# Kernel tuning notes

Measured on AMD Instinct MI355X. Metric: run time of the kernel, lower is better.

## Reference

```python
import jax, jax.numpy as jnp
import numpy as np
import math

FACTOR = 5


def setup_inputs() -> dict:
    key = jax.random.key(0)
    k1, k2, k3, k4 = jax.random.split(key, 4)
    B, L, H, D = 8, 1024, 8, 64
    S = FACTOR * math.ceil(math.log(L))  # U_part = 35
    return {
        "queries": jax.random.normal(k1, (B, L, H, D), jnp.float32),
        "keys": jax.random.normal(k2, (B, L, H, D), jnp.float32),
        "values": jax.random.normal(k3, (B, L, H, D), jnp.float32),
        "sample_idx": jax.random.randint(k4, (L, S), 0, L, dtype=jnp.int32),
        "attn_mask": 0,  # unused by the original forward
    }


def reference(queries, keys, values, sample_idx, attn_mask):
    B, L_Q, H, D = queries.shape
    L_K = keys.shape[1]
    # [B, L, H, D] -> [B, H, L, D]
    Q = jnp.transpose(queries, (0, 2, 1, 3))
    K = jnp.transpose(keys, (0, 2, 1, 3))
    V = jnpp_transpose(values) if False else jnp.transpose(values, (0, 2, 1, 3))

    u = min(FACTOR * math.ceil(math.log(L_Q)), L_Q)  # n_top

    # --- _prob_QK: sampled scores, sparsity measure, top-u query selection ---
    K_sample = K[:, :, sample_idx, :]  # [B, H, L_Q, S, D]
    QK_sample = jnp.einsum('bhqd,bhqsd->bhqs', Q, K_sample)  # [B, H, L_Q, S]
    M = QK_sample.max(axis=-1) - QK_sample.sum(axis=-1) / L_K  # [B, H, L_Q]
    _, M_top = jax.lax.top_k(M, u)  # [B, H, u]

    Q_reduce = jnp.take_along_axis(Q, M_top[..., None], axis=2)  # [B, H, u, D]
    scale = 1.0 / math.sqrt(D)
    scores_top = jnp.einsum('bhud,bhkd->bhuk', Q_reduce, K) * scale  # [B, H, u, L_K]

    # --- initial context (mask_flag=True): running causal mean of V ---
    denom = jnp.arange(1, L_K + 1, dtype=V.dtype)[:, None]  # [L_K, 1]
    context = jnp.cumsum(V, axis=2) / denom  # [B, H, L_K, D]

    # --- softmax over keys, sparse update of selected query rows ---
    attn = jax.nn.softmax(scores_top, axis=-1)  # [B, H, u, L_K]
    update = jnp.einsum('bhuk,bhkd->bhud', attn, V)  # [B, H, u, D]

    b_idx = jnp.arange(B)[:, None, None]
    h_idx = jnp.arange(H)[None, :, None]
    context = context.at[b_idx, h_idx, M_top].set(update)

    return jnp.transpose(context, (0, 2, 1, 3))  # [B, L_Q, H, D]
```

## Files before the change

kernel.cpp:

```cpp
#include <hip/hip_runtime.h>
#include <math.h>

#define BB 8
#define LL 1024
#define HH 8
#define DD 64
#define SS 35
#define UU 35
#define BH (BB*HH)
#define NCHK 4
#define CHK 256
#define RPAD 48

#define CSBLOCKS BH
#define MBLOCKS (BB*LL)

typedef __attribute__((ext_vector_type(8))) short short8;
typedef __attribute__((ext_vector_type(4))) float f32x4;

__device__ __forceinline__ size_t qkv_off(int b, int l, int h, int d) {
    return (((size_t)b*LL + l)*HH + h)*DD + d;
}

__device__ __forceinline__ unsigned short f2bf(float x) {
    unsigned int u = __float_as_uint(x);
    u = (u + 0x7fffu + ((u >> 16) & 1u)) >> 16;
    return (unsigned short)u;
}

__device__ __forceinline__ short8 ld_bf8_g(const float* __restrict__ p) {
    float4 x = *reinterpret_cast<const float4*>(p);
    float4 y = *reinterpret_cast<const float4*>(p + 4);
    short8 r;
    r[0] = (short)f2bf(x.x); r[1] = (short)f2bf(x.y);
    r[2] = (short)f2bf(x.z); r[3] = (short)f2bf(x.w);
    r[4] = (short)f2bf(y.x); r[5] = (short)f2bf(y.y);
    r[6] = (short)f2bf(y.z); r[7] = (short)f2bf(y.w);
    return r;
}

__device__ __forceinline__ void gload_lds16(const void* g, void* l) {
    __builtin_amdgcn_global_load_lds(
        (const __attribute__((address_space(1))) void*)g,
        (__attribute__((address_space(3))) void*)l, 16, 0, 0);
}

__device__ __forceinline__ float red8_shr(float p) {
    int t;
    t = __builtin_amdgcn_update_dpp(0, __float_as_int(p), 0x111, 0xF, 0xF, true);
    p += __int_as_float(t);
    t = __builtin_amdgcn_update_dpp(0, __float_as_int(p), 0x112, 0xF, 0xF, true);
    p += __int_as_float(t);
    t = __builtin_amdgcn_update_dpp(0, __float_as_int(p), 0x114, 0xF, 0xF, true);
    p += __int_as_float(t);
    return p;
}

__device__ __forceinline__ float wave_fmax64(float x) {
    int t;
    t = __builtin_amdgcn_update_dpp(0, __float_as_int(x), 0xB1, 0xF, 0xF, true);
    x = fmaxf(x, __int_as_float(t));
    t = __builtin_amdgcn_update_dpp(0, __float_as_int(x), 0x4E, 0xF, 0xF, true);
    x = fmaxf(x, __int_as_float(t));
    t = __builtin_amdgcn_update_dpp(0, __float_as_int(x), 0x141, 0xF, 0xF, true);
    x = fmaxf(x, __int_as_float(t));
    t = __builtin_amdgcn_update_dpp(0, __float_as_int(x), 0x140, 0xF, 0xF, true);
    x = fmaxf(x, __int_as_float(t));
    x = fmaxf(x, __shfl_xor(x, 16));
    x = fmaxf(x, __shfl_xor(x, 32));
    return x;
}

__device__ __forceinline__ int wave_imin64(int x) {
    int t;
    t = __builtin_amdgcn_update_dpp(0, x, 0xB1, 0xF, 0xF, true);  x = (t < x) ? t : x;
    t = __builtin_amdgcn_update_dpp(0, x, 0x4E, 0xF, 0xF, true);  x = (t < x) ? t : x;
    t = __builtin_amdgcn_update_dpp(0, x, 0x141, 0xF, 0xF, true); x = (t < x) ? t : x;
    t = __builtin_amdgcn_update_dpp(0, x, 0x140, 0xF, 0xF, true); x = (t < x) ? t : x;
    int y;
    y = __shfl_xor(x, 16); x = (y < x) ? y : x;
    y = __shfl_xor(x, 32); x = (y < x) ? y : x;
    return x;
}

__global__ __launch_bounds__(256, 3) void kernel_M_cumsum(const float* __restrict__ Q,
                                                          const float* __restrict__ K,
                                                          const float* __restrict__ V,
                                                          const int*   __restrict__ sidx,
                                                          float* __restrict__ M,
                                                          float* __restrict__ out) {
    int blk = blockIdx.x;
    if (blk < CSBLOCKS) {
        __shared__ float partial[4][64];
        int bh = blk;
        int b = bh >> 3, h = bh & 7;
        int d = threadIdx.x & 63, seg = threadIdx.x >> 6;
        int l0 = seg * 256;
        const float* vp = V + qkv_off(b, l0, h, d);

        float s = 0.f;
#pragma unroll 8
        for (int i = 0; i < 256; i++) s += vp[(size_t)i * (HH * DD)];
        partial[seg][d] = s;
        __syncthreads();
        float run = 0.f;
#pragma unroll
        for (int ss = 0; ss < 3; ss++) {
            float v = partial[ss][d];
            run += (ss < seg) ? v : 0.f;
        }
        float* op = out + qkv_off(b, l0, h, d);
#pragma unroll 8
        for (int i = 0; i < 256; i++) {
            run += vp[(size_t)i * (HH * DD)];
            op[(size_t)i * (HH * DD)] = run / (float)(l0 + i + 1);
        }
    } else {
        __shared__ float rows[4 * 2560];
        __shared__ float s_mx[4][8];
        __shared__ float s_sm[4][8];
        int mblk = blk - CSBLOCKS;
        int b = mblk & 7;
        int q = mblk >> 3;
        int tid = threadIdx.x;
        int w = tid >> 6, lane = tid & 63;
        int h = lane >> 3, j = lane & 7;

        const float* qb = Q + ((size_t)(b * LL + q) * HH + h) * DD + j * 4;
        f32x4 q0 = *reinterpret_cast<const f32x4*>(qb);
        f32x4 q1 = *reinterpret_cast<const f32x4*>(qb + 32);

        const int* sq = sidx + q * SS + w * 9;
        const char* kb = (const char*)(K + (size_t)b * (LL * HH * DD));
        char* region = (char*)(rows + w * 2560);
        const float* region_f = rows + w * 2560;

        float mx = -INFINITY, sm = 0.f;

        {
            int sl[5];
#pragma unroll
            for (int i = 0; i < 5; i++) sl[i] = sq[i];
#pragma unroll
            for (int r = 0; r < 5; r++) {
                const char* gsrc = kb + (size_t)sl[r] * 2048 + lane * 16;
                gload_lds16(gsrc,        region + r * 2048);
                gload_lds16(gsrc + 1024, region + r * 2048 + 1024);
            }
            asm volatile("s_waitcnt vmcnt(0)" ::: "memory");
#pragma unroll
            for (int r = 0; r < 5; r++) {
                const float* rp = region_f + r * 512 + h * 64 + j * 4;
                f32x4 k0 = *reinterpret_cast<const f32x4*>(rp);
                f32x4 k1 = *reinterpret_cast<const f32x4*>(rp + 32);
                float d = q0.x * k0.x + q0.y * k0.y + q0.z * k0.z + q0.w * k0.w
                        + q1.x * k1.x + q1.y * k1.y + q1.z * k1.z + q1.w * k1.w;
                d = red8_shr(d);
                mx = fmaxf(mx, d); sm += d;
            }
            asm volatile("s_waitcnt lgkmcnt(0)" ::: "memory");
        }

        {
            int sl[4];
#pragma unroll
            for (int i = 0; i < 4; i++) {
                int ii = (i == 3 && w == 3) ? 2 : i;
                sl[i] = sq[5 + ii];
            }
#pragma unroll
            for (int r = 0; r < 4; r++) {
                const char* gsrc = kb + (size_t)sl[r] * 2048 + lane * 16;
                gload_lds16(gsrc,        region + r * 2048);
                gload_lds16(gsrc + 1024, region + r * 2048 + 1024);
            }
            asm volatile("s_waitcnt vmcnt(0)" ::: "memory");
#pragma unroll
            for (int r = 0; r < 4; r++) {
                const float* rp = region_f + r * 512 + h * 64 + j * 4;
                f32x4 k0 = *reinterpret_cast<const f32x4*>(rp);
                f32x4 k1 = *reinterpret_cast<const f32x4*>(rp + 32);
                float d = q0.x * k0.x + q0.y * k0.y + q0.z * k0.z + q0.w * k0.w
                        + q1.x * k1.x + q1.y * k1.y + q1.z * k1.z + q1.w * k1.w;
                d = red8_shr(d);
                bool valid = (r < 3) || (w < 3);
                if (valid) { mx = fmaxf(mx, d); sm += d; }
            }
        }

        if (j == 7) { s_mx[w][h] = mx; s_sm[w][h] = sm; }
        __syncthreads();
        if (tid < 8) {
            float m2 = -INFINITY, s2 = 0.f;
#pragma unroll
            for (int ww = 0; ww < 4; ww++) {
                m2 = fmaxf(m2, s_mx[ww][tid]);
                s2 += s_sm[ww][tid];
            }
            M[(b * HH + tid) * LL + q] = m2 - s2 * (1.0f / LL);
        }
    }
}

__global__ __launch_bounds__(64, 4) void kernel_topk(const float* __restrict__ M,
                                                     int* __restrict__ top) {
    int bh = blockIdx.x, lane = threadIdx.x;
    float v[16];
#pragma unroll
    for (int i = 0; i < 16; i++) v[i] = M[bh * LL + i * 64 + lane];

    for (int k = 0; k < UU; k++) {
        float bv = -INFINITY; int bslot = 0;
#pragma unroll
        for (int i = 0; i < 16; i++) {
            if (v[i] > bv) { bv = v[i]; bslot = i; }
        }
        float wm = wave_fmax64(bv);
        int gidx = (bv == wm) ? (bslot * 64 + lane) : 0x7fffffff;
        int widx = wave_imin64(gidx);
        if (lane == 0) top[bh * UU + k] = widx;
        if ((widx & 63) == lane) {
            int slot = widx >> 6;
#pragma unroll
            for (int i = 0; i < 16; i++) if (i == slot) v[i] = -INFINITY;
        }
    }
}

__global__ __launch_bounds__(256) void kernel_attn_part(const float* __restrict__ Q,
                                                        const float* __restrict__ K,
                                                        const float* __restrict__ V,
                                                        const int*   __restrict__ top,
                                                        float* __restrict__ m_ws,
                                                        float* __restrict__ se_ws,
                                                        float* __restrict__ pv_ws) {
    __shared__ unsigned short vt[64 * CHK];
    __shared__ unsigned short p_lds[RPAD * CHK];
    __shared__ float red_m[4][RPAD];
    __shared__ float red_se[4][RPAD];
    __shared__ int   qpos_s[RPAD];

    const int blk = blockIdx.x;
    const int bh  = blk >> 2;
    const int ch  = blk & 3;
    const int b   = bh >> 3, h = bh & 7;
    const int l0  = ch * CHK;
    const int tid = threadIdx.x;
    const int w    = tid >> 6;
    const int lane = tid & 63;
    const int c    = lane & 15;
    const int g    = lane >> 4;
    const float scale = 0.125f;

    if (tid < RPAD) qpos_s[tid] = top[bh * UU + (tid < UU ? tid : UU - 1)];

#pragma unroll
    for (int i = 0; i < 8; i++) {
        int task = i * 256 + tid;
        int d   = task & 63;
        int lq8 = task >> 6;
        float vv[8];
#pragma unroll
        for (int jj = 0; jj < 8; jj++)
            vv[jj] = V[qkv_off(b, l0 + lq8 * 8 + jj, h, d)];
        short8 pk;
#pragma unroll
        for (int jj = 0; jj < 8; jj++) pk[jj] = (short)f2bf(vv[jj]);
        *reinterpret_cast<short8*>(vt + d * CHK + (((lq8 ^ (d & 31)) << 3))) = pk;
    }
    __syncthreads();

    f32x4 acc[3][4];
#pragma unroll
    for (int mt = 0; mt < 3; mt++)
#pragma unroll
        for (int nt = 0; nt < 4; nt++) acc[mt][nt] = (f32x4){0.f, 0.f, 0.f, 0.f};

#pragma unroll
    for (int ks = 0; ks < 2; ks++) {
        int k0 = ks * 32 + g * 8;
        short8 af[3];
#pragma unroll
        for (int mt = 0; mt < 3; mt++) {
            int row = mt * 16 + c;
            af[mt] = ld_bf8_g(Q + qkv_off(b, qpos_s[row], h, k0));
        }
#pragma unroll
        for (int nt = 0; nt < 4; nt++) {
            int kl = l0 + w * 64 + nt * 16 + c;
            short8 bf = ld_bf8_g(K + qkv_off(b, kl, h, k0));
#pragma unroll
            for (int mt = 0; mt < 3; mt++)
                acc[mt][nt] = __builtin_amdgcn_mfma_f32_16x16x32_bf16(af[mt], bf, acc[mt][nt], 0, 0, 0);
        }
    }

    float tmax[3][4];
#pragma unroll
    for (int mt = 0; mt < 3; mt++)
#pragma unroll
        for (int r = 0; r < 4; r++) {
            float m = fmaxf(fmaxf(acc[mt][0][r], acc[mt][1][r]),
                            fmaxf(acc[mt][2][r], acc[mt][3][r]));
            m = fmaxf(m, __shfl_xor(m, 1));
            m = fmaxf(m, __shfl_xor(m, 2));
            m = fmaxf(m, __shfl_xor(m, 4));
            m = fmaxf(m, __shfl_xor(m, 8));
            tmax[mt][r] = m;
        }
    if (c == 0) {
#pragma unroll
        for (int mt = 0; mt < 3; mt++)
#pragma unroll
            for (int r = 0; r < 4; r++)
                red_m[w][mt * 16 + g * 4 + r] = tmax[mt][r];
    }
    __syncthreads();

    float tse[3][4];
#pragma unroll
    for (int mt = 0; mt < 3; mt++)
#pragma unroll
        for (int r = 0; r < 4; r++) {
            int row = mt * 16 + g * 4 + r;
            float m = fmaxf(fmaxf(red_m[0][row], red_m[1][row]),
                            fmaxf(red_m[2][row], red_m[3][row]));
            float s = 0.f;
#pragma unroll
            for (int nt = 0; nt < 4; nt++) {
                float p = __expf(scale * (acc[mt][nt][r] - m));
                acc[mt][nt][r] = p;
                s += p;
                p_lds[row * CHK + w * 64 + nt * 16 + c] = f2bf(p);
            }
            s += __shfl_xor(s, 1);
            s += __shfl_xor(s, 2);
            s += __shfl_xor(s, 4);
            s += __shfl_xor(s, 8);
            tse[mt][r] = s;
        }
    if (c == 0) {
#pragma unroll
        for (int mt = 0; mt < 3; mt++)
#pragma unroll
            for (int r = 0; r < 4; r++)
                red_se[w][mt * 16 + g * 4 + r] = tse[mt][r];
    }
    __syncthreads();

    if (tid < RPAD) {
        float mm = fmaxf(fmaxf(red_m[0][tid], red_m[1][tid]),
                         fmaxf(red_m[2][tid], red_m[3][tid]));
        float ss = red_se[0][tid] + red_se[1][tid] + red_se[2][tid] + red_se[3][tid];
        m_ws[blk * RPAD + tid]  = mm;
        se_ws[blk * RPAD + tid] = ss;
    }

    f32x4 acc2[3];
#pragma unroll
    for (int mt = 0; mt < 3; mt++) acc2[mt] = (f32x4){0.f, 0.f, 0.f, 0.f};

#pragma unroll
    for (int ks = 0; ks < 8; ks++) {
        int slot = ks * 4 + g;
        int d    = w * 16 + c;
        short8 bf = *reinterpret_cast<const short8*>(
            vt + d * CHK + ((slot ^ (d & 31)) << 3));
#pragma unroll
        for (int mt = 0; mt < 3; mt++) {
            short8 af = *reinterpret_cast<const short8*>(
                p_lds + (mt * 16 + c) * CHK + ks * 32 + g * 8);
            acc2[mt] = __builtin_amdgcn_mfma_f32_16x16x32_bf16(af, bf, acc2[mt], 0, 0, 0);
        }
    }

#pragma unroll
    for (int mt = 0; mt < 3; mt++)
#pragma unroll
        for (int r = 0; r < 4; r++) {
            int row = mt * 16 + g * 4 + r;
            pv_ws[((size_t)blk * RPAD + row) * 64 + w * 16 + c] = acc2[mt][r];
        }
}

__global__ __launch_bounds__(256) void kernel_attn_comb(const int* __restrict__ top,
                                                        const float* __restrict__ m_ws,
                                                        const float* __restrict__ se_ws,
                                                        const float* __restrict__ pv_ws,
                                                        float* __restrict__ out) {
    int bh = blockIdx.x;
    int b = bh >> 3, h = bh & 7;
    const float scale = 0.125f;
    for (int idx = threadIdx.x; idx < UU * 64; idx += 256) {
        int r = idx >> 6, d = idx & 63;
        float mc[NCHK];
        float mm = -INFINITY;
#pragma unroll
        for (int ch = 0; ch < NCHK; ch++) {
            mc[ch] = m_ws[(bh * NCHK + ch) * RPAD + r];
            mm = fmaxf(mm, mc[ch]);
        }
        float num = 0.f, den = 0.f;
#pragma unroll
        for (int ch = 0; ch < NCHK; ch++) {
            float f = __expf(scale * (mc[ch] - mm));
            num += f * pv_ws[((size_t)(bh * NCHK + ch) * RPAD + r) * 64 + d];
            den += f * se_ws[(bh * NCHK + ch) * RPAD + r];
        }
        out[qkv_off(b, top[bh * UU + r], h, d)] = num / den;
    }
}

extern "C" void kernel_launch(void* const* d_in, const int* in_sizes, int n_in,
                              void* d_out, int out_size, void* d_ws, size_t ws_size,
                              hipStream_t stream) {
    const float* Q    = (const float*)d_in[0];
    const float* K    = (const float*)d_in[1];
    const float* V    = (const float*)d_in[2];
    const int*   sidx = (const int*)d_in[3];
    float* out = (float*)d_out;

    char* ws = (char*)d_ws;
    float* M     = (float*)(ws);
    int*   top   = (int*)  (ws + 262144);
    float* m_ws  = (float*)(ws + 272384);
    float* se_ws = (float*)(ws + 321536);
    float* pv_ws = (float*)(ws + 370688);

    kernel_M_cumsum <<<CSBLOCKS + MBLOCKS, 256, 0, stream>>>(Q, K, V, sidx, M, out);
    kernel_topk     <<<BH, 64, 0, stream>>>(M, top);
    kernel_attn_part<<<BH * NCHK, 256, 0, stream>>>(Q, K, V, top, m_ws, se_ws, pv_ws);
    kernel_attn_comb<<<BH, 256, 0, stream>>>(top, m_ws, se_ws, pv_ws, out);
}
```

Measured before the change: 75.93 us.

## Shrink LDS staging to 3-row batches with XOR swizzle to raise occupancy

The sampled-QK part of the fused kernel now stages K rows in three batches of three rows instead of five plus four. This cuts per-block shared memory from 40 KB to 24 KB and raises launch_bounds min blocks from 3 to 6. It also XOR-swizzles the global-to-LDS copy source offsets and the matching LDS read addresses to avoid bank conflicts on the 16-byte reads. The cost is one extra load/wait round per wave, which means less memory-level parallelism per block.

```diff
diff --git a/kernel.cpp b/kernel.cpp
--- a/kernel.cpp
+++ b/kernel.cpp
@@ -83,7 +83,7 @@
     return x;
 }
 
-__global__ __launch_bounds__(256, 3) void kernel_M_cumsum(const float* __restrict__ Q,
+__global__ __launch_bounds__(256, 6) void kernel_M_cumsum(const float* __restrict__ Q,
                                                           const float* __restrict__ K,
                                                           const float* __restrict__ V,
                                                           const int*   __restrict__ sidx,
@@ -116,7 +116,7 @@
             op[(size_t)i * (HH * DD)] = run / (float)(l0 + i + 1);
         }
     } else {
-        __shared__ float rows[4 * 2560];
+        __shared__ float rows[4 * 1536];
         __shared__ float s_mx[4][8];
         __shared__ float s_sm[4][8];
         int mblk = blk - CSBLOCKS;
@@ -132,60 +132,44 @@
 
         const int* sq = sidx + q * SS + w * 9;
         const char* kb = (const char*)(K + (size_t)b * (LL * HH * DD));
-        char* region = (char*)(rows + w * 2560);
-        const float* region_f = rows + w * 2560;
+        char* region = (char*)(rows + w * 1536);
+        const float* region_f = rows + w * 1536;
+
+        int srcA = (lane ^ ((lane >> 4) & 7)) << 4;
+        int srcB = 1024 + ((lane ^ (4 | (lane >> 4))) << 4);
+        int ps1 = ((h << 4) + j) ^ h;
+        int ps2 = ((h << 4) + j + 8) ^ h;
 
         float mx = -INFINITY, sm = 0.f;
 
-        {
-            int sl[5];
-#pragma unroll
-            for (int i = 0; i < 5; i++) sl[i] = sq[i];
-#pragma unroll
-            for (int r = 0; r < 5; r++) {
-                const char* gsrc = kb + (size_t)sl[r] * 2048 + lane * 16;
-                gload_lds16(gsrc,        region + r * 2048);
-                gload_lds16(gsrc + 1024, region + r * 2048 + 1024);
+#pragma unroll
+        for (int batch = 0; batch < 3; batch++) {
+            int sl[3];
+#pragma unroll
+            for (int i = 0; i < 3; i++) {
+                int s = batch * 3 + i;
+                int ii = (s == 8 && w == 3) ? 7 : s;
+                sl[i] = sq[ii];
+            }
+#pragma unroll
+            for (int r = 0; r < 3; r++) {
+                const char* gsrc = kb + (size_t)sl[r] * 2048;
+                gload_lds16(gsrc + srcA, region + r * 2048);
+                gload_lds16(gsrc + srcB, region + r * 2048 + 1024);
             }
             asm volatile("s_waitcnt vmcnt(0)" ::: "memory");
 #pragma unroll
-            for (int r = 0; r < 5; r++) {
-                const float* rp = region_f + r * 512 + h * 64 + j * 4;
-                f32x4 k0 = *reinterpret_cast<const f32x4*>(rp);
-                f32x4 k1 = *reinterpret_cast<const f32x4*>(rp + 32);
+            for (int r = 0; r < 3; r++) {
+                const float* rp = region_f + r * 512;
+                f32x4 k0 = *reinterpret_cast<const f32x4*>(rp + ps1 * 4);
+                f32x4 k1 = *reinterpret_cast<const f32x4*>(rp + ps2 * 4);
                 float d = q0.x * k0.x + q0.y * k0.y + q0.z * k0.z + q0.w * k0.w
                         + q1.x * k1.x + q1.y * k1.y + q1.z * k1.z + q1.w * k1.w;
                 d = red8_shr(d);
-                mx = fmaxf(mx, d); sm += d;
+                bool valid = (batch * 3 + r < 8) || (w < 3);
+                if (valid) { mx = fmaxf(mx, d); sm += d; }
             }
             asm volatile("s_waitcnt lgkmcnt(0)" ::: "memory");
-        }
-
-        {
-            int sl[4];
-#pragma unroll
-            for (int i = 0; i < 4; i++) {
-                int ii = (i == 3 && w == 3) ? 2 : i;
-                sl[i] = sq[5 + ii];
-            }
-#pragma unroll
-            for (int r = 0; r < 4; r++) {
-                const char* gsrc = kb + (size_t)sl[r] * 2048 + lane * 16;
-                gload_lds16(gsrc,        region + r * 2048);
-                gload_lds16(gsrc + 1024, region + r * 2048 + 1024);
-            }
-            asm volatile("s_waitcnt vmcnt(0)" ::: "memory");
-#pragma unroll
-            for (int r = 0; r < 4; r++) {
-                const float* rp = region_f + r * 512 + h * 64 + j * 4;
-                f32x4 k0 = *reinterpret_cast<const f32x4*>(rp);
-                f32x4 k1 = *reinterpret_cast<const f32x4*>(rp + 32);
-                float d = q0.x * k0.x + q0.y * k0.y + q0.z * k0.z + q0.w * k0.w
-                        + q1.x * k1.x + q1.y * k1.y + q1.z * k1.z + q1.w * k1.w;
-                d = red8_shr(d);
-                bool valid = (r < 3) || (w < 3);
-                if (valid) { mx = fmaxf(mx, d); sm += d; }
-            }
         }
 
         if (j == 7) { s_mx[w][h] = mx; s_sm[w][h] = sm; }
```

Measured after the change: 79.45 us. 1.05x slower.
